# Kernel tuning notes

Measured on AMD Instinct MI355X. Metric: run time of the kernel, lower is better.

## Reference

```python
import jax, jax.numpy as jnp
import numpy as np

NUM_HEADS = 8
SR_RATIO = 2
LN_EPS = 1e-5


def setup_inputs() -> dict:
    key = jax.random.key(0)
    ks = jax.random.split(key, 8)
    B, N, C = 8, 4096, 512
    s = 0.02  # weight init scale to keep logits sane
    return {
        "x": jax.random.normal(ks[0], (B, N, C), jnp.float32),
        "q_w": jax.random.normal(ks[1], (C, C), jnp.float32) * s,
        "q_b": jnp.zeros((C,), jnp.float32),
        "kv_w": jax.random.normal(ks[2], (2 * C, C), jnp.float32) * s,
        "kv_b": jnp.zeros((2 * C,), jnp.float32),
        "sr_w": jax.random.normal(ks[3], (C, C, SR_RATIO, SR_RATIO), jnp.float32) * s,
        "sr_b": jnp.zeros((C,), jnp.float32),
        "ln_g": jnp.ones((C,), jnp.float32),
        "ln_b": jnp.zeros((C,), jnp.float32),
        "proj_w": jax.random.normal(ks[4], (C, C), jnp.float32) * s,
        "proj_b": jnp.zeros((C,), jnp.float32),
        "H": 64,
        "W": 64,
    }


def _layernorm(x, g, b):
    mu = jnp.mean(x, axis=-1, keepdims=True)
    var = jnp.var(x, axis=-1, keepdims=True)
    return (x - mu) * jax.lax.rsqrt(var + LN_EPS) * g + b


def reference(x, q_w, q_b, kv_w, kv_b, sr_w, sr_b, ln_g, ln_b, proj_w, proj_b, H, W):
    B, N, C = x.shape
    h = NUM_HEADS
    d = C // h
    scale = d ** (-0.5)

    # q: [B, h, N, d]
    q = (x @ q_w.T + q_b).reshape(B, N, h, d).transpose(0, 2, 1, 3)

    # spatial reduction: Conv2d(C, C, k=SR, stride=SR) on [B, C, H, W]
    x_img = x.transpose(0, 2, 1).reshape(B, C, H, W)
    x_sr = jax.lax.conv_general_dilated(
        x_img, sr_w,
        window_strides=(SR_RATIO, SR_RATIO), padding="VALID",
        dimension_numbers=("NCHW", "OIHW", "NCHW"),
    ) + sr_b[None, :, None, None]
    N2 = (H // SR_RATIO) * (W // SR_RATIO)
    x_sr = x_sr.reshape(B, C, N2).transpose(0, 2, 1)  # [B, N2, C]
    x_sr = _layernorm(x_sr, ln_g, ln_b)

    # kv: [2, B, h, N2, d]
    kv = (x_sr @ kv_w.T + kv_b).reshape(B, N2, 2, h, d).transpose(2, 0, 3, 1, 4)
    k, v = kv[0], kv[1]

    attn = jax.nn.softmax(jnp.einsum("bhnd,bhmd->bhnm", q, k) * scale, axis=-1)
    out = jnp.einsum("bhnm,bhmd->bhnd", attn, v)  # [B, h, N, d]
    out = out.transpose(0, 2, 1, 3).reshape(B, N, C)
    return out @ proj_w.T + proj_b
```

## Files before the change

kernel.cpp:

```cpp
#include <hip/hip_runtime.h>
#include <hip/hip_bf16.h>

typedef __hip_bfloat16 bf16;
typedef __bf16 bf16x8 __attribute__((ext_vector_type(8)));
typedef float f32x16 __attribute__((ext_vector_type(16)));
typedef unsigned int u32;
typedef unsigned int u32x2 __attribute__((ext_vector_type(2)));

typedef const __attribute__((address_space(1))) void GV;
typedef __attribute__((address_space(3))) void LV;

#define TM 128
#define TN 128
#define TK 64

static __device__ __forceinline__ float fexp2(float x) {
#if __has_builtin(__builtin_amdgcn_exp2f)
    return __builtin_amdgcn_exp2f(x);
#else
    return exp2f(x);
#endif
}

__global__ void prep_k(const float* __restrict__ x, const float* __restrict__ qw,
                       const float* __restrict__ kvw, const float* __restrict__ pjw,
                       const float* __restrict__ srw,
                       bf16* __restrict__ xb, bf16* __restrict__ qwb,
                       bf16* __restrict__ kvwb, bf16* __restrict__ pjwb,
                       bf16* __restrict__ srwb) {
    const int bid = blockIdx.x;
    const int tid = threadIdx.x;
    if (bid < 17408) {
        const float* src;
        bf16* dst;
        int i;
        if (bid < 16384)      { src = x;   dst = xb;   i = bid * 256 + tid; }
        else if (bid < 16640) { src = qw;  dst = qwb;  i = (bid - 16384) * 256 + tid; }
        else if (bid < 17152) { src = kvw; dst = kvwb; i = (bid - 16640) * 256 + tid; }
        else                  { src = pjw; dst = pjwb; i = (bid - 17152) * 256 + tid; }
        float4 a = reinterpret_cast<const float4*>(src)[i];
        bf16* d = dst + (size_t)i * 4;
        d[0] = __float2bfloat16(a.x);
        d[1] = __float2bfloat16(a.y);
        d[2] = __float2bfloat16(a.z);
        d[3] = __float2bfloat16(a.w);
    } else {
        int idx = (bid - 17408) * 256 + tid;
        int co = idx >> 11;
        int t  = idx & 2047;
        int p  = t >> 9;
        int ci = t & 511;
        srwb[idx] = __float2bfloat16(srw[(size_t)co * 2048 + ci * 4 + p]);
    }
}

template<int KIND>
__device__ __forceinline__ void gemm_body(int bid, bf16* ldsA, bf16* ldsB,
                                          const bf16* __restrict__ A, const bf16* __restrict__ Bw,
                                          const float* __restrict__ bias,
                                          bf16* __restrict__ outB, bf16* __restrict__ outB2,
                                          float* __restrict__ outF, int N, int K) {
    const int tid = threadIdx.x;
    const int lane = tid & 63;
    const int wave = tid >> 6;
    const int ntn = N / TN;
    const int row0 = (bid / ntn) * TM;
    const int col0 = (bid % ntn) * TN;
    const int wm = wave >> 1, wn = wave & 1;
    const int l31 = lane & 31;
    const int hi8 = lane >> 5;
    const int NK = K / TK;

    f32x16 acc[2][2];
#pragma unroll
    for (int i = 0; i < 2; ++i)
#pragma unroll
        for (int j = 0; j < 2; ++j) acc[i][j] = f32x16{};

    for (int ks = 0; ks < NK; ++ks) {
        const int k0 = ks * TK;
#pragma unroll
        for (int t = 0; t < 4; ++t) {
            int idx = t * 256 + tid;
            int r = idx >> 3;
            int c = ((idx & 7) ^ (r & 7)) * 8;
            const bf16* src;
            if (KIND == 1) {
                int rr = row0 + r;
                int k = k0 + c;
                int p = k >> 9, ci = k & 511;
                int b = rr >> 10, ii = (rr >> 5) & 31, jj = rr & 31;
                int n_in = (2 * ii + (p >> 1)) * 64 + 2 * jj + (p & 1);
                src = A + ((size_t)(b * 4096 + n_in)) * 512 + ci;
            } else {
                src = A + (size_t)(row0 + r) * K + k0 + c;
            }
            __builtin_amdgcn_global_load_lds((GV*)src, (LV*)&ldsA[idx * 8], 16, 0, 0);
        }
#pragma unroll
        for (int t = 0; t < 4; ++t) {
            int idx = t * 256 + tid;
            int r = idx >> 3;
            int c = ((idx & 7) ^ (r & 7)) * 8;
            const bf16* src = Bw + (size_t)(col0 + r) * K + k0 + c;
            __builtin_amdgcn_global_load_lds((GV*)src, (LV*)&ldsB[idx * 8], 16, 0, 0);
        }
        __syncthreads();

#pragma unroll
        for (int kk = 0; kk < 4; ++kk) {
            bf16x8 af[2], bfr[2];
#pragma unroll
            for (int m = 0; m < 2; ++m) {
                int row = wm * 64 + m * 32 + l31;
                int chunk = (kk * 2 + hi8) ^ (row & 7);
                af[m] = *reinterpret_cast<const bf16x8*>(&ldsA[row * 64 + chunk * 8]);
            }
#pragma unroll
            for (int n = 0; n < 2; ++n) {
                int row = wn * 64 + n * 32 + l31;
                int chunk = (kk * 2 + hi8) ^ (row & 7);
                bfr[n] = *reinterpret_cast<const bf16x8*>(&ldsB[row * 64 + chunk * 8]);
            }
#pragma unroll
            for (int m = 0; m < 2; ++m)
#pragma unroll
                for (int n = 0; n < 2; ++n)
                    acc[m][n] = __builtin_amdgcn_mfma_f32_32x32x16_bf16(af[m], bfr[n], acc[m][n], 0, 0, 0);
        }
        __syncthreads();
    }

#pragma unroll
    for (int m = 0; m < 2; ++m) {
#pragma unroll
        for (int n = 0; n < 2; ++n) {
#pragma unroll
            for (int r = 0; r < 16; ++r) {
                int grow = row0 + wm * 64 + m * 32 + (r & 3) + 8 * (r >> 2) + 4 * (lane >> 5);
                int gcol = col0 + wn * 64 + n * 32 + l31;
                float v = acc[m][n][r] + bias[gcol];
                if (KIND == 0) {
                    int b = grow >> 12, nn = grow & 4095;
                    int h = gcol >> 6, dd = gcol & 63;
                    outB[(((size_t)(b * 8 + h)) * 4096 + nn) * 64 + dd] =
                        __float2bfloat16(v * 0.18033688011112042f);
                } else if (KIND == 1) {
                    outF[(size_t)grow * 512 + gcol] = v;
                } else if (KIND == 2) {
                    int b = grow >> 10, mm = grow & 1023;
                    if (gcol < 512) {
                        int h = gcol >> 6, dd = gcol & 63;
                        outB[(((size_t)(b * 8 + h)) * 1024 + mm) * 64 + dd] = __float2bfloat16(v);
                    } else {
                        int c2 = gcol - 512;
                        int h = c2 >> 6, dd = c2 & 63;
                        outB2[(((size_t)(b * 8 + h)) * 64 + dd) * 1024 + mm] = __float2bfloat16(v);
                    }
                } else {
                    outF[(size_t)grow * 512 + gcol] = v;
                }
            }
        }
    }
}

__launch_bounds__(256, 3)
__global__ void gemm01_k(const bf16* __restrict__ xb, const bf16* __restrict__ qw,
                         const bf16* __restrict__ srw, const float* __restrict__ q_b,
                         const float* __restrict__ sr_b,
                         bf16* __restrict__ q_out, float* __restrict__ xsr_out) {
    __shared__ __align__(16) bf16 ldsA[TM * TK];
    __shared__ __align__(16) bf16 ldsB[TM * TK];
    if (blockIdx.x < 256)
        gemm_body<1>(blockIdx.x, ldsA, ldsB, xb, srw, sr_b,
                     nullptr, nullptr, xsr_out, 512, 2048);
    else
        gemm_body<0>(blockIdx.x - 256, ldsA, ldsB, xb, qw, q_b,
                     q_out, nullptr, nullptr, 512, 512);
}

__launch_bounds__(256, 3)
__global__ void gemm2_k(const bf16* __restrict__ A, const bf16* __restrict__ Bw,
                        const float* __restrict__ bias,
                        bf16* __restrict__ kout, bf16* __restrict__ vtout) {
    __shared__ __align__(16) bf16 ldsA[TM * TK];
    __shared__ __align__(16) bf16 ldsB[TM * TK];
    gemm_body<2>(blockIdx.x, ldsA, ldsB, A, Bw, bias, kout, vtout, nullptr, 1024, 512);
}

__launch_bounds__(256, 3)
__global__ void gemm3_k(const bf16* __restrict__ A, const bf16* __restrict__ Bw,
                        const float* __restrict__ bias, float* __restrict__ outF) {
    __shared__ __align__(16) bf16 ldsA[TM * TK];
    __shared__ __align__(16) bf16 ldsB[TM * TK];
    gemm_body<3>(blockIdx.x, ldsA, ldsB, A, Bw, bias, nullptr, nullptr, outF, 512, 512);
}

__global__ void ln_k(const float* __restrict__ xsr, const float* __restrict__ g,
                     const float* __restrict__ bta, bf16* __restrict__ out) {
    const int row = blockIdx.x;
    const int tid = threadIdx.x;
    const float* xr = xsr + (size_t)row * 512;
    float2 v = *reinterpret_cast<const float2*>(xr + tid * 2);
    float s = v.x + v.y;
    float sq = v.x * v.x + v.y * v.y;
#pragma unroll
    for (int m = 1; m < 64; m <<= 1) {
        s += __shfl_xor(s, m, 64);
        sq += __shfl_xor(sq, m, 64);
    }
    __shared__ float rs[4], rq[4];
    int wave = tid >> 6, lane = tid & 63;
    if (lane == 0) { rs[wave] = s; rq[wave] = sq; }
    __syncthreads();
    s = rs[0] + rs[1] + rs[2] + rs[3];
    sq = rq[0] + rq[1] + rq[2] + rq[3];
    float mu = s * (1.f / 512.f);
    float var = sq * (1.f / 512.f) - mu * mu;
    float rstd = rsqrtf(var + 1e-5f);
    bf16* orow = out + (size_t)row * 512;
    orow[tid * 2]     = __float2bfloat16((v.x - mu) * rstd * g[tid * 2] + bta[tid * 2]);
    orow[tid * 2 + 1] = __float2bfloat16((v.y - mu) * rstd * g[tid * 2 + 1] + bta[tid * 2 + 1]);
}

__launch_bounds__(256, 4)
__global__ void attn_k(const bf16* __restrict__ Q, const bf16* __restrict__ Kb,
                       const bf16* __restrict__ Vt, bf16* __restrict__ Out) {
    const int p = blockIdx.x;
    const int bh = (p & 7) * 8 + (p >> 8);
    const int qb = (p >> 3) & 31;
    const int b = bh >> 3, h = bh & 7;
    const int tid = threadIdx.x, lane = tid & 63, wave = tid >> 6;
    const int q0 = qb * 128 + wave * 32;
    const int l31 = lane & 31;
    const int klo8 = (lane >> 5) * 8;

    const bf16* Qp = Q + ((size_t)bh * 4096 + q0) * 64;
    const bf16* Kp = Kb + (size_t)bh * 1024 * 64;
    const bf16* Vp = Vt + (size_t)bh * 64 * 1024;

    __shared__ __align__(16) char smem[32768];

    bf16x8 qf[4];
#pragma unroll
    for (int c = 0; c < 4; ++c)
        qf[c] = *reinterpret_cast<const bf16x8*>(Qp + (size_t)l31 * 64 + c * 16 + klo8);

    f32x16 accO[2];
    accO[0] = f32x16{};
    accO[1] = f32x16{};
    f32x16 accL = f32x16{};
    const f32x16 z16 = f32x16{};

    union { u32 u[4]; bf16x8 v; } onesu;
    onesu.u[0] = 0x3F803F80u; onesu.u[1] = 0x3F803F80u;
    onesu.u[2] = 0x3F803F80u; onesu.u[3] = 0x3F803F80u;
    const bf16x8 ones8 = onesu.v;

    const int l2 = lane >> 1;
    const int lh8 = (lane & 1) * 8;
    const int w16 = wave * 16;

    const char* rb = smem + l31 * 32 + (lane >> 5) * 16;

#define STAGE_TILE(KT, BASE)                                                              \
    do {                                                                                  \
        char* _b = (BASE);                                                                \
        __builtin_amdgcn_global_load_lds((GV*)(Kp + (size_t)((KT) + l2) * 64 + w16 + lh8),\
                                         (LV*)(_b + wave * 2048), 16, 0, 0);              \
        __builtin_amdgcn_global_load_lds((GV*)(Kp + (size_t)((KT) + 32 + l2) * 64 + w16 + lh8),\
                                         (LV*)(_b + wave * 2048 + 1024), 16, 0, 0);       \
        __builtin_amdgcn_global_load_lds((GV*)(Vp + (size_t)l2 * 1024 + (KT) + w16 + lh8),\
                                         (LV*)(_b + 8192 + wave * 2048), 16, 0, 0);       \
        __builtin_amdgcn_global_load_lds((GV*)(Vp + (size_t)(32 + l2) * 1024 + (KT) + w16 + lh8),\
                                         (LV*)(_b + 8192 + wave * 2048 + 1024), 16, 0, 0);\
    } while (0)

    STAGE_TILE(0, smem);
    STAGE_TILE(64, smem + 16384);

    int cur = 0;
    for (int t = 0; t < 16; ++t) {
        if (t < 15) asm volatile("s_waitcnt vmcnt(4)" ::: "memory");
        else        asm volatile("s_waitcnt vmcnt(0)" ::: "memory");
        __builtin_amdgcn_s_barrier();

        const char* rc = rb + cur * 16384;

        bf16x8 kf0[4], kf1[4];
#pragma unroll
        for (int c = 0; c < 4; ++c) {
            kf0[c] = *reinterpret_cast<const bf16x8*>(rc + c * 2048);
            kf1[c] = *reinterpret_cast<const bf16x8*>(rc + c * 2048 + 1024);
        }
        f32x16 sA = __builtin_amdgcn_mfma_f32_32x32x16_bf16(kf0[0], qf[0], z16, 0, 0, 0);
        f32x16 sB = __builtin_amdgcn_mfma_f32_32x32x16_bf16(kf1[0], qf[0], z16, 0, 0, 0);
#pragma unroll
        for (int c = 1; c < 4; ++c) {
            sA = __builtin_amdgcn_mfma_f32_32x32x16_bf16(kf0[c], qf[c], sA, 0, 0, 0);
            sB = __builtin_amdgcn_mfma_f32_32x32x16_bf16(kf1[c], qf[c], sB, 0, 0, 0);
        }

        float pA[16], pB[16];
#pragma unroll
        for (int r = 0; r < 16; ++r) pA[r] = fexp2(sA[r]);
#pragma unroll
        for (int r = 0; r < 16; ++r) pB[r] = fexp2(sB[r]);

        u32 wA[8], wB[8];
#pragma unroll
        for (int k = 0; k < 8; ++k) {
            union { __hip_bfloat162 h2; u32 u; } cv;
            cv.h2 = __float22bfloat162_rn(float2{pA[2 * k], pA[2 * k + 1]});
            wA[k] = cv.u;
            union { __hip_bfloat162 h2; u32 u; } cw;
            cw.h2 = __float22bfloat162_rn(float2{pB[2 * k], pB[2 * k + 1]});
            wB[k] = cw.u;
        }
        union { u32 u[4]; bf16x8 v; } fr[4];
        {
            u32x2 e0 = __builtin_amdgcn_permlane32_swap(wA[0], wA[2], false, false);
            u32x2 e1 = __builtin_amdgcn_permlane32_swap(wA[1], wA[3], false, false);
            fr[0].u[0] = e0[0]; fr[0].u[1] = e1[0]; fr[0].u[2] = e0[1]; fr[0].u[3] = e1[1];
            u32x2 e2 = __builtin_amdgcn_permlane32_swap(wA[4], wA[6], false, false);
            u32x2 e3 = __builtin_amdgcn_permlane32_swap(wA[5], wA[7], false, false);
            fr[1].u[0] = e2[0]; fr[1].u[1] = e3[0]; fr[1].u[2] = e2[1]; fr[1].u[3] = e3[1];
            u32x2 e4 = __builtin_amdgcn_permlane32_swap(wB[0], wB[2], false, false);
            u32x2 e5 = __builtin_amdgcn_permlane32_swap(wB[1], wB[3], false, false);
            fr[2].u[0] = e4[0]; fr[2].u[1] = e5[0]; fr[2].u[2] = e4[1]; fr[2].u[3] = e5[1];
            u32x2 e6 = __builtin_amdgcn_permlane32_swap(wB[4], wB[6], false, false);
            u32x2 e7 = __builtin_amdgcn_permlane32_swap(wB[5], wB[7], false, false);
            fr[3].u[0] = e6[0]; fr[3].u[1] = e7[0]; fr[3].u[2] = e6[1]; fr[3].u[3] = e7[1];
        }

        __builtin_amdgcn_s_setprio(1);
#pragma unroll
        for (int dd = 0; dd < 2; ++dd) {
#pragma unroll
            for (int kk = 0; kk < 4; ++kk) {
                bf16x8 vv = *reinterpret_cast<const bf16x8*>(rc + 8192 + kk * 2048 + dd * 1024);
                accO[dd] = __builtin_amdgcn_mfma_f32_32x32x16_bf16(vv, fr[kk].v, accO[dd], 0, 0, 0);
            }
        }
#pragma unroll
        for (int kk = 0; kk < 4; ++kk)
            accL = __builtin_amdgcn_mfma_f32_32x32x16_bf16(ones8, fr[kk].v, accL, 0, 0, 0);
        __builtin_amdgcn_s_setprio(0);

        __builtin_amdgcn_s_barrier();
        if (t + 2 < 16) STAGE_TILE((t + 2) * 64, smem + cur * 16384);
        cur ^= 1;
    }

    __syncthreads();

    typedef bf16 (*ObufT)[32][72];
    ObufT obuf = (ObufT)smem;
    float inv = 1.f / accL[0];
#pragma unroll
    for (int dd = 0; dd < 2; ++dd)
#pragma unroll
        for (int r = 0; r < 16; r += 2) {
            int d = dd * 32 + (r & 3) + 8 * (r >> 2) + 4 * (lane >> 5);
            union { __hip_bfloat162 h2; u32 u; } cv;
            cv.h2 = __float22bfloat162_rn(float2{accO[dd][r] * inv, accO[dd][r + 1] * inv});
            *reinterpret_cast<u32*>(&obuf[wave][l31][d]) = cv.u;
        }
    __syncthreads();
    {
        int qr = lane >> 1, hf = lane & 1;
        const bf16* orow = &obuf[wave][qr][hf * 32];
        bf16* gout = Out + ((size_t)b * 4096 + q0 + qr) * 512 + h * 64 + hf * 32;
#pragma unroll
        for (int j = 0; j < 4; ++j) {
            bf16x8 t2 = *reinterpret_cast<const bf16x8*>(orow + j * 8);
            *reinterpret_cast<bf16x8*>(gout + j * 8) = t2;
        }
    }
#undef STAGE_TILE
}

extern "C" void kernel_launch(void* const* d_in, const int* in_sizes, int n_in,
                              void* d_out, int out_size, void* d_ws, size_t ws_size,
                              hipStream_t stream) {
    const float* x      = (const float*)d_in[0];
    const float* q_w    = (const float*)d_in[1];
    const float* q_b    = (const float*)d_in[2];
    const float* kv_w   = (const float*)d_in[3];
    const float* kv_b   = (const float*)d_in[4];
    const float* sr_w   = (const float*)d_in[5];
    const float* sr_b   = (const float*)d_in[6];
    const float* ln_g   = (const float*)d_in[7];
    const float* ln_b   = (const float*)d_in[8];
    const float* proj_w = (const float*)d_in[9];
    const float* proj_b = (const float*)d_in[10];

    char* w = (char*)d_ws;
    bf16* x_bf   = (bf16*)w; w += (size_t)8 * 4096 * 512 * 2;
    bf16* q_bf   = (bf16*)w; w += (size_t)8 * 4096 * 512 * 2;
    bf16* qw_bf  = (bf16*)w; w += (size_t)512 * 512 * 2;
    bf16* kvw_bf = (bf16*)w; w += (size_t)1024 * 512 * 2;
    bf16* srw_bf = (bf16*)w; w += (size_t)512 * 2048 * 2;
    bf16* pjw_bf = (bf16*)w; w += (size_t)512 * 512 * 2;
    float* xsr_f = (float*)w; w += (size_t)8 * 1024 * 512 * 4;
    bf16* xsrb   = (bf16*)w; w += (size_t)8 * 1024 * 512 * 2;
    bf16* k_bf   = (bf16*)w; w += (size_t)8 * 8 * 1024 * 64 * 2;
    bf16* vt_bf  = (bf16*)w; w += (size_t)8 * 8 * 1024 * 64 * 2;
    bf16* ao_bf  = (bf16*)w; w += (size_t)8 * 4096 * 512 * 2;

    prep_k<<<dim3(21504), dim3(256), 0, stream>>>(x, q_w, kv_w, proj_w, sr_w,
                                                  x_bf, qw_bf, kvw_bf, pjw_bf, srw_bf);

    gemm01_k<<<dim3(1280), dim3(256), 0, stream>>>(x_bf, qw_bf, srw_bf, q_b, sr_b, q_bf, xsr_f);
    ln_k<<<dim3(8192), dim3(256), 0, stream>>>(xsr_f, ln_g, ln_b, xsrb);
    gemm2_k<<<dim3(512), dim3(256), 0, stream>>>(xsrb, kvw_bf, kv_b, k_bf, vt_bf);
    attn_k<<<dim3(2048), dim3(256), 0, stream>>>(q_bf, k_bf, vt_bf, ao_bf);
    gemm3_k<<<dim3(1024), dim3(256), 0, stream>>>(ao_bf, pjw_bf, proj_b, (float*)d_out);
}
```

Baseline: 234.9 us.

## Triple-buffer attention K/V tiles and swizzle GEMM block order

The attention kernel moves from double to triple buffering of K/V tiles in shared memory. The prefetch for tile t+2 is now issued right after the top barrier, which removes the second barrier per iteration. This costs 48KB of LDS per block, so the occupancy hint drops from 4 to 3 blocks. The GEMM kernels also remap block indices with a stride-8 interleave, likely to match the chiplet/XCD round-robin dispatch and improve L2 reuse of shared tiles.

```diff
diff --git a/kernel.cpp b/kernel.cpp
--- a/kernel.cpp
+++ b/kernel.cpp
@@ -172,12 +172,15 @@
                          bf16* __restrict__ q_out, float* __restrict__ xsr_out) {
     __shared__ __align__(16) bf16 ldsA[TM * TK];
     __shared__ __align__(16) bf16 ldsB[TM * TK];
-    if (blockIdx.x < 256)
-        gemm_body<1>(blockIdx.x, ldsA, ldsB, xb, srw, sr_b,
-                     nullptr, nullptr, xsr_out, 512, 2048);
-    else
-        gemm_body<0>(blockIdx.x - 256, ldsA, ldsB, xb, qw, q_b,
-                     q_out, nullptr, nullptr, 512, 512);
+    const int p = blockIdx.x;
+    if (p < 256) {
+        int s = (p & 7) * 32 + (p >> 3);
+        gemm_body<1>(s, ldsA, ldsB, xb, srw, sr_b, nullptr, nullptr, xsr_out, 512, 2048);
+    } else {
+        int p2 = p - 256;
+        int s = (p2 & 7) * 128 + (p2 >> 3);
+        gemm_body<0>(s, ldsA, ldsB, xb, qw, q_b, q_out, nullptr, nullptr, 512, 512);
+    }
 }
 
 __launch_bounds__(256, 3)
@@ -186,7 +189,8 @@
                         bf16* __restrict__ kout, bf16* __restrict__ vtout) {
     __shared__ __align__(16) bf16 ldsA[TM * TK];
     __shared__ __align__(16) bf16 ldsB[TM * TK];
-    gemm_body<2>(blockIdx.x, ldsA, ldsB, A, Bw, bias, kout, vtout, nullptr, 1024, 512);
+    int s = (blockIdx.x & 7) * 64 + (blockIdx.x >> 3);
+    gemm_body<2>(s, ldsA, ldsB, A, Bw, bias, kout, vtout, nullptr, 1024, 512);
 }
 
 __launch_bounds__(256, 3)
@@ -194,7 +198,8 @@
                         const float* __restrict__ bias, float* __restrict__ outF) {
     __shared__ __align__(16) bf16 ldsA[TM * TK];
     __shared__ __align__(16) bf16 ldsB[TM * TK];
-    gemm_body<3>(blockIdx.x, ldsA, ldsB, A, Bw, bias, nullptr, nullptr, outF, 512, 512);
+    int s = (blockIdx.x & 7) * 128 + (blockIdx.x >> 3);
+    gemm_body<3>(s, ldsA, ldsB, A, Bw, bias, nullptr, nullptr, outF, 512, 512);
 }
 
 __global__ void ln_k(const float* __restrict__ xsr, const float* __restrict__ g,
@@ -224,7 +229,7 @@
     orow[tid * 2 + 1] = __float2bfloat16((v.y - mu) * rstd * g[tid * 2 + 1] + bta[tid * 2 + 1]);
 }
 
-__launch_bounds__(256, 4)
+__launch_bounds__(256, 3)
 __global__ void attn_k(const bf16* __restrict__ Q, const bf16* __restrict__ Kb,
                        const bf16* __restrict__ Vt, bf16* __restrict__ Out) {
     const int p = blockIdx.x;
@@ -240,7 +245,7 @@
     const bf16* Kp = Kb + (size_t)bh * 1024 * 64;
     const bf16* Vp = Vt + (size_t)bh * 64 * 1024;
 
-    __shared__ __align__(16) char smem[32768];
+    __shared__ __align__(16) char smem[49152];
 
     bf16x8 qf[4];
 #pragma unroll
@@ -261,8 +266,7 @@
     const int l2 = lane >> 1;
     const int lh8 = (lane & 1) * 8;
     const int w16 = wave * 16;
-
-    const char* rb = smem + l31 * 32 + (lane >> 5) * 16;
+    const int roff = l31 * 32 + (lane >> 5) * 16;
 
 #define STAGE_TILE(KT, BASE)                                                              \
     do {                                                                                  \
@@ -277,16 +281,19 @@
                                          (LV*)(_b + 8192 + wave * 2048 + 1024), 16, 0, 0);\
     } while (0)
 
-    STAGE_TILE(0, smem);
-    STAGE_TILE(64, smem + 16384);
-
-    int cur = 0;
+    char* bA = smem;
+    char* bB = smem + 16384;
+    char* bC = smem + 32768;
+    STAGE_TILE(0, bA);
+    STAGE_TILE(64, bB);
+
     for (int t = 0; t < 16; ++t) {
         if (t < 15) asm volatile("s_waitcnt vmcnt(4)" ::: "memory");
         else        asm volatile("s_waitcnt vmcnt(0)" ::: "memory");
         __builtin_amdgcn_s_barrier();
-
-        const char* rc = rb + cur * 16384;
+        if (t + 2 < 16) STAGE_TILE((t + 2) * 64, bC);
+
+        const char* rc = bA + roff;
 
         bf16x8 kf0[4], kf1[4];
 #pragma unroll
@@ -348,9 +355,7 @@
             accL = __builtin_amdgcn_mfma_f32_32x32x16_bf16(ones8, fr[kk].v, accL, 0, 0, 0);
         __builtin_amdgcn_s_setprio(0);
 
-        __builtin_amdgcn_s_barrier();
-        if (t + 2 < 16) STAGE_TILE((t + 2) * 64, smem + cur * 16384);
-        cur ^= 1;
+        char* tmp = bA; bA = bB; bB = bC; bC = tmp;
     }
 
     __syncthreads();
```

Measured after the change: 217.7 us. 7.4% less time.
